# Optimization experiments

Hardware: AMD Instinct MI355X
Metric: run time of the kernel (lower is better)

## Reference

```python
import jax, jax.numpy as jnp
import numpy as np

HIDDEN = 128

def setup_inputs() -> dict:
    key = jax.random.key(0)
    ks = jax.random.split(key, 7)
    B, T, I, O = 256, 512, 256, 1000
    s_ih = 1.0 / np.sqrt(HIDDEN)
    x = jax.random.normal(ks[0], (B, T, I), dtype=jnp.float32)
    W_ih = jax.random.uniform(ks[1], (HIDDEN, I), minval=-s_ih, maxval=s_ih, dtype=jnp.float32)
    W_hh = jax.random.uniform(ks[2], (HIDDEN, HIDDEN), minval=-s_ih, maxval=s_ih, dtype=jnp.float32)
    b_ih = jax.random.uniform(ks[3], (HIDDEN,), minval=-s_ih, maxval=s_ih, dtype=jnp.float32)
    b_hh = jax.random.uniform(ks[4], (HIDDEN,), minval=-s_ih, maxval=s_ih, dtype=jnp.float32)
    s_fc = 1.0 / np.sqrt(HIDDEN)
    W_fc = jax.random.uniform(ks[5], (O, HIDDEN), minval=-s_fc, maxval=s_fc, dtype=jnp.float32)
    b_fc = jax.random.uniform(ks[6], (O,), minval=-s_fc, maxval=s_fc, dtype=jnp.float32)
    return {"x": x, "W_ih": W_ih, "W_hh": W_hh, "b_ih": b_ih, "b_hh": b_hh, "W_fc": W_fc, "b_fc": b_fc}


def reference(x, W_ih, W_hh, b_ih, b_hh, W_fc, b_fc):
    B = x.shape[0]
    # Precompute input projection for all timesteps in one big GEMM: [B,T,H]
    xp = jnp.einsum('bti,hi->bth', x, W_ih) + b_ih + b_hh
    h0 = jnp.zeros((B, HIDDEN), dtype=x.dtype)

    def step(h, xp_t):
        h = jnp.tanh(xp_t + h @ W_hh.T)
        return h, None

    # scan over time axis; only the final hidden state feeds the fc head
    h_last, _ = jax.lax.scan(step, h0, jnp.swapaxes(xp, 0, 1))
    return h_last @ W_fc.T + b_fc
```

## Files before the change

### kernel.cpp

```cpp
#include <hip/hip_runtime.h>


#define HID    128
#define TSTEPS 512
#define BATCH  256
#define INDIM  256
#define ODIM   1000

typedef _Float16 f16x8 __attribute__((ext_vector_type(8)));
typedef __fp16   fp16x2 __attribute__((ext_vector_type(2)));
typedef float    f32x4 __attribute__((ext_vector_type(4)));

__device__ __forceinline__ unsigned pk16(float a, float b) {
    union { fp16x2 h; unsigned u; } t;
    t.h = __builtin_amdgcn_cvt_pkrtz(a, b);
    return t.u;
}
__device__ __forceinline__ float tanh_fast(float v) {
    float e = __expf(2.f * v);
    float r = __builtin_amdgcn_rcpf(e + 1.f);
    return __builtin_fmaf(-2.f, r, 1.f);
}

__global__ __launch_bounds__(256) void k_phase1(const float* __restrict__ x,
                                                const float* __restrict__ Wih,
                                                const float* __restrict__ bih,
                                                const float* __restrict__ bhh,
                                                float* __restrict__ xp) {
    __shared__ __align__(16) _Float16 xs[2][4096];
    __shared__ __align__(16) _Float16 wsm[2][4096];

    const int tid  = threadIdx.x;
    const int wave = tid >> 6, lane = tid & 63;
    const int quad = lane >> 4, l16 = lane & 15;
    const int wm = wave >> 1, wn = wave & 1;
    const int m0 = blockIdx.x * 128;

    int srow[4], scol[4], sdst[4];
#pragma unroll
    for (int q = 0; q < 4; q++) {
        int li = q * 256 + tid;
        srow[q] = li >> 3;
        scol[q] = li & 7;
        sdst[q] = srow[q] * 32 + ((((scol[q] >> 1) ^ srow[q]) & 3) << 3) + ((scol[q] & 1) << 2);
    }

    f32x4 bias_v[4];
#pragma unroll
    for (int nt = 0; nt < 4; nt++) {
        int j0 = wn * 64 + nt * 16 + quad * 4;
        bias_v[nt] = *(const f32x4*)(bih + j0) + *(const f32x4*)(bhh + j0);
    }

    float4 rx[4], rw[4];
#define LOAD_STAGE(KC)                                                              \
    {                                                                               \
        _Pragma("unroll") for (int q = 0; q < 4; q++) {                             \
            rx[q] = *(const float4*)(x + (size_t)(m0 + srow[q]) * INDIM + (KC) * 32 + scol[q] * 4); \
            rw[q] = *(const float4*)(Wih + (size_t)srow[q] * INDIM + (KC) * 32 + scol[q] * 4);      \
        }                                                                           \
    }
#define WRITE_STAGE(BUF)                                                            \
    {                                                                               \
        _Pragma("unroll") for (int q = 0; q < 4; q++) {                             \
            uint2 px, pw;                                                           \
            px.x = pk16(rx[q].x, rx[q].y); px.y = pk16(rx[q].z, rx[q].w);           \
            pw.x = pk16(rw[q].x, rw[q].y); pw.y = pk16(rw[q].z, rw[q].w);           \
            *(uint2*)&xs[BUF][sdst[q]]  = px;                                       \
            *(uint2*)&wsm[BUF][sdst[q]] = pw;                                       \
        }                                                                           \
    }

    f32x4 acc[4][4];
#pragma unroll
    for (int mt = 0; mt < 4; mt++)
#pragma unroll
        for (int nt = 0; nt < 4; nt++) {
            acc[mt][nt].x = 0.f; acc[mt][nt].y = 0.f;
            acc[mt][nt].z = 0.f; acc[mt][nt].w = 0.f;
        }

    LOAD_STAGE(0);
    WRITE_STAGE(0);
    __syncthreads();

    for (int kc = 0; kc < 8; kc++) {
        const int b = kc & 1;
        if (kc < 7) LOAD_STAGE(kc + 1);

        f16x8 a[4], bw[4];
#pragma unroll
        for (int mt = 0; mt < 4; mt++) {
            int row = wm * 64 + mt * 16 + l16;
            a[mt] = *(const f16x8*)&xs[b][row * 32 + (((quad ^ row) & 3) << 3)];
        }
#pragma unroll
        for (int nt = 0; nt < 4; nt++) {
            int row = wn * 64 + nt * 16 + l16;
            bw[nt] = *(const f16x8*)&wsm[b][row * 32 + (((quad ^ row) & 3) << 3)];
        }
#pragma unroll
        for (int mt = 0; mt < 4; mt++)
#pragma unroll
            for (int nt = 0; nt < 4; nt++)
                acc[mt][nt] = __builtin_amdgcn_mfma_f32_16x16x32_f16(bw[nt], a[mt], acc[mt][nt], 0, 0, 0);

        if (kc < 7) WRITE_STAGE(b ^ 1);
        __syncthreads();
    }

#pragma unroll
    for (int mt = 0; mt < 4; mt++) {
        int row = m0 + wm * 64 + mt * 16 + l16;
#pragma unroll
        for (int nt = 0; nt < 4; nt++) {
            int col = wn * 64 + nt * 16 + quad * 4;
            *(f32x4*)&xp[(size_t)row * HID + col] = acc[mt][nt] + bias_v[nt];
        }
    }
#undef LOAD_STAGE
#undef WRITE_STAGE
}

#define RNN_STEP4(TV, XQI, XQC, PB) {                                             \
    uint2 pw;                                                                     \
    pw.x = pk16(tanh_fast(C.x), tanh_fast(C.y));                                  \
    pw.y = pk16(tanh_fast(C.z), tanh_fast(C.w));                                  \
    *(uint2*)&hp[PB][waddr] = pw;                                                 \
    if ((TV) + 4 < TSTEPS)                                                        \
        XQI = *(const f32x4*)(xpb + ((TV) + 4) * HID);                            \
    asm volatile("s_waitcnt lgkmcnt(0)\n\ts_barrier" ::: "memory");               \
    f16x8 H0 = *(const f16x8*)&hp[PB][raddr0];                                    \
    f16x8 H1 = *(const f16x8*)&hp[PB][raddr1];                                    \
    f16x8 H2 = *(const f16x8*)&hp[PB][raddr2];                                    \
    f16x8 H3 = *(const f16x8*)&hp[PB][raddr3];                                    \
    f32x4 ch = XQC, cl;                                                           \
    cl.x = 0.f; cl.y = 0.f; cl.z = 0.f; cl.w = 0.f;                               \
    ch = __builtin_amdgcn_mfma_f32_16x16x32_f16(Wf[0], H0, ch, 0, 0, 0);          \
    cl = __builtin_amdgcn_mfma_f32_16x16x32_f16(Wf[2], H2, cl, 0, 0, 0);          \
    ch = __builtin_amdgcn_mfma_f32_16x16x32_f16(Wf[1], H1, ch, 0, 0, 0);          \
    cl = __builtin_amdgcn_mfma_f32_16x16x32_f16(Wf[3], H3, cl, 0, 0, 0);          \
    C = ch + cl;                                                                  \
}

__global__ __launch_bounds__(512) void k_rnn4(const float* __restrict__ Whh,
                                              float* __restrict__ ws) {
    __shared__ __align__(16) _Float16 hp[2][16 * 128];
    const int tid  = threadIdx.x;
    const int wave = tid >> 6, lane = tid & 63;
    const int quad = lane >> 4, l16 = lane & 15;
    const int r0   = blockIdx.x * 16;

    f16x8 Wf[4];
#pragma unroll
    for (int kc = 0; kc < 4; kc++) {
        const float* p = Whh + (size_t)(16 * wave + l16) * HID + kc * 32 + quad * 8;
        float4 e0 = *(const float4*)p, e1 = *(const float4*)(p + 4);
        union { unsigned u[4]; f16x8 v; } t;
        t.u[0] = pk16(e0.x, e0.y); t.u[1] = pk16(e0.z, e0.w);
        t.u[2] = pk16(e1.x, e1.y); t.u[3] = pk16(e1.z, e1.w);
        Wf[kc] = t.v;
    }

    const int raddr0 = l16 * 128 + ((((0 * 4 + quad) ^ l16) & 15) << 3);
    const int raddr1 = l16 * 128 + ((((1 * 4 + quad) ^ l16) & 15) << 3);
    const int raddr2 = l16 * 128 + ((((2 * 4 + quad) ^ l16) & 15) << 3);
    const int raddr3 = l16 * 128 + ((((3 * 4 + quad) ^ l16) & 15) << 3);
    const int waddr  = l16 * 128 + ((((2 * wave + (quad >> 1)) ^ l16) & 15) << 3) + ((quad & 1) << 2);

    const float* xpb = ws + (size_t)(r0 + l16) * (TSTEPS * HID) + 16 * wave + 4 * quad;

    f32x4 C, xq0, xq1, xq2, xq3;
    C   = *(const f32x4*)(xpb);
    xq1 = *(const f32x4*)(xpb + 1 * HID);
    xq2 = *(const f32x4*)(xpb + 2 * HID);
    xq3 = *(const f32x4*)(xpb + 3 * HID);

    for (int t = 0; t < 508; t += 4) {
        RNN_STEP4(t,     xq0, xq1, 0);
        RNN_STEP4(t + 1, xq1, xq2, 1);
        RNN_STEP4(t + 2, xq2, xq3, 0);
        RNN_STEP4(t + 3, xq3, xq0, 1);
    }
    RNN_STEP4(508, xq0, xq1, 0);
    RNN_STEP4(509, xq1, xq2, 1);
    RNN_STEP4(510, xq2, xq3, 0);

    f32x4 o;
    o.x = tanh_fast(C.x); o.y = tanh_fast(C.y);
    o.z = tanh_fast(C.z); o.w = tanh_fast(C.w);
    *(f32x4*)(ws + (size_t)(r0 + l16) * (TSTEPS * HID) + 16 * wave + 4 * quad) = o;
}
#undef RNN_STEP4

__global__ __launch_bounds__(256) void k_fc(const float* __restrict__ ws,
                                            const float* __restrict__ Wfc,
                                            const float* __restrict__ bfc,
                                            float* __restrict__ out) {
    __shared__ float hb[HID];
    const int b   = blockIdx.x;
    const int tid = threadIdx.x;
    if (tid < HID) hb[tid] = ws[(size_t)b * (TSTEPS * HID) + tid];
    __syncthreads();

    for (int o = tid; o < ODIM; o += 256) {
        const float* wr = Wfc + (size_t)o * HID;
        float acc = 0.f;
#pragma unroll
        for (int q = 0; q < 32; q++) {
            float4 wv = *(const float4*)(wr + q * 4);
            float4 hv = *(const float4*)&hb[q * 4];
            acc += wv.x * hv.x + wv.y * hv.y + wv.z * hv.z + wv.w * hv.w;
        }
        out[(size_t)b * ODIM + o] = acc + bfc[o];
    }
}

extern "C" void kernel_launch(void* const* d_in, const int* in_sizes, int n_in,
                              void* d_out, int out_size, void* d_ws, size_t ws_size,
                              hipStream_t stream) {
    const float* x   = (const float*)d_in[0];
    const float* Wih = (const float*)d_in[1];
    const float* Whh = (const float*)d_in[2];
    const float* bih = (const float*)d_in[3];
    const float* bhh = (const float*)d_in[4];
    const float* Wfc = (const float*)d_in[5];
    const float* bfc = (const float*)d_in[6];
    float* out = (float*)d_out;
    float* ws  = (float*)d_ws;

    k_phase1<<<dim3(1024), dim3(256), 0, stream>>>(x, Wih, bih, bhh, ws);
    k_rnn4  <<<dim3(16),   dim3(512), 0, stream>>>(Whh, ws);
    k_fc    <<<dim3(BATCH), dim3(256), 0, stream>>>(ws, Wfc, bfc, out);
}
```

Before: 375.4 us.

## Fuse input projection and recurrence with staged atomic counters and fp16 workspace

Merges the input-projection GEMM and the recurrent scan into one launch. Sixteen blocks run the recurrence while the remaining blocks compute the projection in four time-ordered stages, each signalled through a global atomic counter, so the scan can start before the full GEMM finishes. The projected activations are also stored in fp16 rather than fp32, halving workspace traffic. The cost is reduced precision of the precomputed inputs, and the spin-wait relies on all recurrence blocks being co-resident with the producers, which risks stalls or deadlock if scheduling does not cooperate.

```diff
diff --git a/kernel.cpp b/kernel.cpp
--- a/kernel.cpp
+++ b/kernel.cpp
@@ -22,134 +22,133 @@
     return __builtin_fmaf(-2.f, r, 1.f);
 }
 
-__global__ __launch_bounds__(256) void k_phase1(const float* __restrict__ x,
-                                                const float* __restrict__ Wih,
-                                                const float* __restrict__ bih,
-                                                const float* __restrict__ bhh,
-                                                float* __restrict__ xp) {
+#define CTR_OFF (33u << 20)
+
+__global__ void k_zero(float* ws) {
+    int* ctr = (int*)((char*)ws + CTR_OFF);
+    if (threadIdx.x < 4) ctr[threadIdx.x] = 0;
+}
+
+
+__global__ __launch_bounds__(512) void k_fused(const float* __restrict__ x,
+                                               const float* __restrict__ Wih,
+                                               const float* __restrict__ bih,
+                                               const float* __restrict__ bhh,
+                                               const float* __restrict__ Whh,
+                                               float* __restrict__ ws) {
     __shared__ __align__(16) _Float16 xs[2][4096];
     __shared__ __align__(16) _Float16 wsm[2][4096];
+    __shared__ __align__(16) _Float16 hp[2][16 * 128];
 
     const int tid  = threadIdx.x;
     const int wave = tid >> 6, lane = tid & 63;
     const int quad = lane >> 4, l16 = lane & 15;
-    const int wm = wave >> 1, wn = wave & 1;
-    const int m0 = blockIdx.x * 128;
-
-    int srow[4], scol[4], sdst[4];
-#pragma unroll
-    for (int q = 0; q < 4; q++) {
-        int li = q * 256 + tid;
-        srow[q] = li >> 3;
-        scol[q] = li & 7;
-        sdst[q] = srow[q] * 32 + ((((scol[q] >> 1) ^ srow[q]) & 3) << 3) + ((scol[q] & 1) << 2);
-    }
-
-    f32x4 bias_v[4];
-#pragma unroll
-    for (int nt = 0; nt < 4; nt++) {
-        int j0 = wn * 64 + nt * 16 + quad * 4;
-        bias_v[nt] = *(const f32x4*)(bih + j0) + *(const f32x4*)(bhh + j0);
-    }
-
-    float4 rx[4], rw[4];
+    int* ctr = (int*)((char*)ws + CTR_OFF);
+    _Float16* xp16 = (_Float16*)ws;
+
+    if (blockIdx.x >= 16) {
+        const int pb    = blockIdx.x - 16;
+        const int stage = pb >> 8;
+        const int m0    = ((pb & 255) * 4 + stage) * 128;
+        const int wm = wave >> 1, wn = wave & 1;
+
+        int srow[2], scol[2], sdst[2];
+#pragma unroll
+        for (int q = 0; q < 2; q++) {
+            int li = q * 512 + tid;
+            srow[q] = li >> 3;
+            scol[q] = li & 7;
+            sdst[q] = srow[q] * 32 + ((((scol[q] >> 1) ^ srow[q]) & 3) << 3) + ((scol[q] & 1) << 2);
+        }
+
+        f32x4 bias_v[4];
+#pragma unroll
+        for (int nt = 0; nt < 4; nt++) {
+            int j0 = wn * 64 + nt * 16 + quad * 4;
+            bias_v[nt] = *(const f32x4*)(bih + j0) + *(const f32x4*)(bhh + j0);
+        }
+
+        float4 rx[2], rw[2];
 #define LOAD_STAGE(KC)                                                              \
-    {                                                                               \
-        _Pragma("unroll") for (int q = 0; q < 4; q++) {                             \
-            rx[q] = *(const float4*)(x + (size_t)(m0 + srow[q]) * INDIM + (KC) * 32 + scol[q] * 4); \
-            rw[q] = *(const float4*)(Wih + (size_t)srow[q] * INDIM + (KC) * 32 + scol[q] * 4);      \
-        }                                                                           \
-    }
+        {                                                                           \
+            _Pragma("unroll") for (int q = 0; q < 2; q++) {                         \
+                rx[q] = *(const float4*)(x + (size_t)(m0 + srow[q]) * INDIM + (KC) * 32 + scol[q] * 4); \
+                rw[q] = *(const float4*)(Wih + (size_t)srow[q] * INDIM + (KC) * 32 + scol[q] * 4);      \
+            }                                                                       \
+        }
 #define WRITE_STAGE(BUF)                                                            \
-    {                                                                               \
-        _Pragma("unroll") for (int q = 0; q < 4; q++) {                             \
-            uint2 px, pw;                                                           \
-            px.x = pk16(rx[q].x, rx[q].y); px.y = pk16(rx[q].z, rx[q].w);           \
-            pw.x = pk16(rw[q].x, rw[q].y); pw.y = pk16(rw[q].z, rw[q].w);           \
-            *(uint2*)&xs[BUF][sdst[q]]  = px;                                       \
-            *(uint2*)&wsm[BUF][sdst[q]] = pw;                                       \
-        }                                                                           \
-    }
-
-    f32x4 acc[4][4];
-#pragma unroll
-    for (int mt = 0; mt < 4; mt++)
-#pragma unroll
-        for (int nt = 0; nt < 4; nt++) {
-            acc[mt][nt].x = 0.f; acc[mt][nt].y = 0.f;
-            acc[mt][nt].z = 0.f; acc[mt][nt].w = 0.f;
-        }
-
-    LOAD_STAGE(0);
-    WRITE_STAGE(0);
-    __syncthreads();
-
-    for (int kc = 0; kc < 8; kc++) {
-        const int b = kc & 1;
-        if (kc < 7) LOAD_STAGE(kc + 1);
-
-        f16x8 a[4], bw[4];
-#pragma unroll
-        for (int mt = 0; mt < 4; mt++) {
-            int row = wm * 64 + mt * 16 + l16;
-            a[mt] = *(const f16x8*)&xs[b][row * 32 + (((quad ^ row) & 3) << 3)];
-        }
-#pragma unroll
-        for (int nt = 0; nt < 4; nt++) {
-            int row = wn * 64 + nt * 16 + l16;
-            bw[nt] = *(const f16x8*)&wsm[b][row * 32 + (((quad ^ row) & 3) << 3)];
-        }
-#pragma unroll
-        for (int mt = 0; mt < 4; mt++)
-#pragma unroll
-            for (int nt = 0; nt < 4; nt++)
-                acc[mt][nt] = __builtin_amdgcn_mfma_f32_16x16x32_f16(bw[nt], a[mt], acc[mt][nt], 0, 0, 0);
-
-        if (kc < 7) WRITE_STAGE(b ^ 1);
+        {                                                                           \
+            _Pragma("unroll") for (int q = 0; q < 2; q++) {                         \
+                uint2 px, pw;                                                       \
+                px.x = pk16(rx[q].x, rx[q].y); px.y = pk16(rx[q].z, rx[q].w);       \
+                pw.x = pk16(rw[q].x, rw[q].y); pw.y = pk16(rw[q].z, rw[q].w);       \
+                *(uint2*)&xs[BUF][sdst[q]]  = px;                                   \
+                *(uint2*)&wsm[BUF][sdst[q]] = pw;                                   \
+            }                                                                       \
+        }
+
+        f32x4 acc[2][4];
+#pragma unroll
+        for (int mt = 0; mt < 2; mt++)
+#pragma unroll
+            for (int nt = 0; nt < 4; nt++) {
+                acc[mt][nt].x = 0.f; acc[mt][nt].y = 0.f;
+                acc[mt][nt].z = 0.f; acc[mt][nt].w = 0.f;
+            }
+
+        LOAD_STAGE(0);
+        WRITE_STAGE(0);
         __syncthreads();
-    }
-
-#pragma unroll
-    for (int mt = 0; mt < 4; mt++) {
-        int row = m0 + wm * 64 + mt * 16 + l16;
-#pragma unroll
-        for (int nt = 0; nt < 4; nt++) {
-            int col = wn * 64 + nt * 16 + quad * 4;
-            *(f32x4*)&xp[(size_t)row * HID + col] = acc[mt][nt] + bias_v[nt];
-        }
-    }
+
+        for (int kc = 0; kc < 8; kc++) {
+            const int b = kc & 1;
+            if (kc < 7) LOAD_STAGE(kc + 1);
+
+            f16x8 a[2], bw[4];
+#pragma unroll
+            for (int mt = 0; mt < 2; mt++) {
+                int row = wm * 32 + mt * 16 + l16;
+                a[mt] = *(const f16x8*)&xs[b][row * 32 + (((quad ^ row) & 3) << 3)];
+            }
+#pragma unroll
+            for (int nt = 0; nt < 4; nt++) {
+                int row = wn * 64 + nt * 16 + l16;
+                bw[nt] = *(const f16x8*)&wsm[b][row * 32 + (((quad ^ row) & 3) << 3)];
+            }
+#pragma unroll
+            for (int mt = 0; mt < 2; mt++)
+#pragma unroll
+                for (int nt = 0; nt < 4; nt++)
+                    acc[mt][nt] = __builtin_amdgcn_mfma_f32_16x16x32_f16(bw[nt], a[mt], acc[mt][nt], 0, 0, 0);
+
+            if (kc < 7) WRITE_STAGE(b ^ 1);
+            __syncthreads();
+        }
+
+#pragma unroll
+        for (int mt = 0; mt < 2; mt++) {
+            int row = m0 + wm * 32 + mt * 16 + l16;
+#pragma unroll
+            for (int nt = 0; nt < 4; nt++) {
+                int col = wn * 64 + nt * 16 + quad * 4;
+                f32x4 v = acc[mt][nt] + bias_v[nt];
+                uint2 p;
+                p.x = pk16(v.x, v.y); p.y = pk16(v.z, v.w);
+                *(uint2*)&xp16[(size_t)row * HID + col] = p;
+            }
+        }
 #undef LOAD_STAGE
 #undef WRITE_STAGE
-}
-
-#define RNN_STEP4(TV, XQI, XQC, PB) {                                             \
-    uint2 pw;                                                                     \
-    pw.x = pk16(tanh_fast(C.x), tanh_fast(C.y));                                  \
-    pw.y = pk16(tanh_fast(C.z), tanh_fast(C.w));                                  \
-    *(uint2*)&hp[PB][waddr] = pw;                                                 \
-    if ((TV) + 4 < TSTEPS)                                                        \
-        XQI = *(const f32x4*)(xpb + ((TV) + 4) * HID);                            \
-    asm volatile("s_waitcnt lgkmcnt(0)\n\ts_barrier" ::: "memory");               \
-    f16x8 H0 = *(const f16x8*)&hp[PB][raddr0];                                    \
-    f16x8 H1 = *(const f16x8*)&hp[PB][raddr1];                                    \
-    f16x8 H2 = *(const f16x8*)&hp[PB][raddr2];                                    \
-    f16x8 H3 = *(const f16x8*)&hp[PB][raddr3];                                    \
-    f32x4 ch = XQC, cl;                                                           \
-    cl.x = 0.f; cl.y = 0.f; cl.z = 0.f; cl.w = 0.f;                               \
-    ch = __builtin_amdgcn_mfma_f32_16x16x32_f16(Wf[0], H0, ch, 0, 0, 0);          \
-    cl = __builtin_amdgcn_mfma_f32_16x16x32_f16(Wf[2], H2, cl, 0, 0, 0);          \
-    ch = __builtin_amdgcn_mfma_f32_16x16x32_f16(Wf[1], H1, ch, 0, 0, 0);          \
-    cl = __builtin_amdgcn_mfma_f32_16x16x32_f16(Wf[3], H3, cl, 0, 0, 0);          \
-    C = ch + cl;                                                                  \
-}
-
-__global__ __launch_bounds__(512) void k_rnn4(const float* __restrict__ Whh,
-                                              float* __restrict__ ws) {
-    __shared__ __align__(16) _Float16 hp[2][16 * 128];
-    const int tid  = threadIdx.x;
-    const int wave = tid >> 6, lane = tid & 63;
-    const int quad = lane >> 4, l16 = lane & 15;
-    const int r0   = blockIdx.x * 16;
+
+        __syncthreads();
+        if (tid == 0) {
+            __threadfence();
+            atomicAdd(&ctr[stage], 1);
+        }
+        return;
+    }
+
+    const int r0 = blockIdx.x * 16;
 
     f16x8 Wf[4];
 #pragma unroll
@@ -168,30 +167,102 @@
     const int raddr3 = l16 * 128 + ((((3 * 4 + quad) ^ l16) & 15) << 3);
     const int waddr  = l16 * 128 + ((((2 * wave + (quad >> 1)) ^ l16) & 15) << 3) + ((quad & 1) << 2);
 
-    const float* xpb = ws + (size_t)(r0 + l16) * (TSTEPS * HID) + 16 * wave + 4 * quad;
-
-    f32x4 C, xq0, xq1, xq2, xq3;
-    C   = *(const f32x4*)(xpb);
-    xq1 = *(const f32x4*)(xpb + 1 * HID);
-    xq2 = *(const f32x4*)(xpb + 2 * HID);
-    xq3 = *(const f32x4*)(xpb + 3 * HID);
-
-    for (int t = 0; t < 508; t += 4) {
+    const _Float16* xpb = xp16 + (size_t)(r0 + l16) * (TSTEPS * HID) + 16 * wave + 4 * quad;
+
+#define WAITSTAGE(S)                                                                \
+    {                                                                               \
+        if (tid == 0) {                                                             \
+            long iv = 0;                                                            \
+            while (__hip_atomic_load(&ctr[S], __ATOMIC_ACQUIRE,                     \
+                                     __HIP_MEMORY_SCOPE_AGENT) < 256 &&             \
+                   ++iv < 200000000L) {}                                            \
+        }                                                                           \
+        __syncthreads();                                                            \
+        __threadfence();                                                            \
+    }
+
+#define CVT4(DST, SRC)                                                              \
+    {                                                                               \
+        union { uint2 u; _Float16 h[4]; } cv_; cv_.u = (SRC);                       \
+        DST.x = (float)cv_.h[0]; DST.y = (float)cv_.h[1];                           \
+        DST.z = (float)cv_.h[2]; DST.w = (float)cv_.h[3];                           \
+    }
+
+#define RNN_STEP4(TV, XQI, XQC, PB) {                                             \
+    uint2 pw;                                                                     \
+    pw.x = pk16(tanh_fast(C.x), tanh_fast(C.y));                                  \
+    pw.y = pk16(tanh_fast(C.z), tanh_fast(C.w));                                  \
+    *(uint2*)&hp[PB][waddr] = pw;                                                 \
+    if ((TV) + 4 < TSTEPS)                                                        \
+        XQI = *(const uint2*)(xpb + (size_t)((TV) + 4) * HID);                    \
+    asm volatile("s_waitcnt lgkmcnt(0)\n\ts_barrier" ::: "memory");               \
+    f32x4 ch; CVT4(ch, XQC);                        \
+    f16x8 H0 = *(const f16x8*)&hp[PB][raddr0];                                    \
+    f16x8 H1 = *(const f16x8*)&hp[PB][raddr1];                                    \
+    f16x8 H2 = *(const f16x8*)&hp[PB][raddr2];                                    \
+    f16x8 H3 = *(const f16x8*)&hp[PB][raddr3];                                    \
+    f32x4 cl;                                                                     \
+    cl.x = 0.f; cl.y = 0.f; cl.z = 0.f; cl.w = 0.f;                               \
+    ch = __builtin_amdgcn_mfma_f32_16x16x32_f16(Wf[0], H0, ch, 0, 0, 0);          \
+    cl = __builtin_amdgcn_mfma_f32_16x16x32_f16(Wf[2], H2, cl, 0, 0, 0);          \
+    ch = __builtin_amdgcn_mfma_f32_16x16x32_f16(Wf[1], H1, ch, 0, 0, 0);          \
+    cl = __builtin_amdgcn_mfma_f32_16x16x32_f16(Wf[3], H3, cl, 0, 0, 0);          \
+    C = ch + cl;                                                                  \
+}
+
+    WAITSTAGE(0);
+
+    f32x4 C;
+    uint2 xq0, xq1, xq2, xq3;
+    {
+        uint2 c0 = *(const uint2*)(xpb);
+        CVT4(C, c0);
+    }
+    xq1 = *(const uint2*)(xpb + 1 * HID);
+    xq2 = *(const uint2*)(xpb + 2 * HID);
+    xq3 = *(const uint2*)(xpb + 3 * HID);
+
+    for (int t = 0; t < 124; t += 4) {
         RNN_STEP4(t,     xq0, xq1, 0);
         RNN_STEP4(t + 1, xq1, xq2, 1);
         RNN_STEP4(t + 2, xq2, xq3, 0);
         RNN_STEP4(t + 3, xq3, xq0, 1);
     }
+    WAITSTAGE(1);
+    for (int t = 124; t < 252; t += 4) {
+        RNN_STEP4(t,     xq0, xq1, 0);
+        RNN_STEP4(t + 1, xq1, xq2, 1);
+        RNN_STEP4(t + 2, xq2, xq3, 0);
+        RNN_STEP4(t + 3, xq3, xq0, 1);
+    }
+    WAITSTAGE(2);
+    for (int t = 252; t < 380; t += 4) {
+        RNN_STEP4(t,     xq0, xq1, 0);
+        RNN_STEP4(t + 1, xq1, xq2, 1);
+        RNN_STEP4(t + 2, xq2, xq3, 0);
+        RNN_STEP4(t + 3, xq3, xq0, 1);
+    }
+    WAITSTAGE(3);
+    for (int t = 380; t < 508; t += 4) {
+        RNN_STEP4(t,     xq0, xq1, 0);
+        RNN_STEP4(t + 1, xq1, xq2, 1);
+        RNN_STEP4(t + 2, xq2, xq3, 0);
+        RNN_STEP4(t + 3, xq3, xq0, 1);
+    }
     RNN_STEP4(508, xq0, xq1, 0);
     RNN_STEP4(509, xq1, xq2, 1);
     RNN_STEP4(510, xq2, xq3, 0);
 
-    f32x4 o;
-    o.x = tanh_fast(C.x); o.y = tanh_fast(C.y);
-    o.z = tanh_fast(C.z); o.w = tanh_fast(C.w);
-    *(f32x4*)(ws + (size_t)(r0 + l16) * (TSTEPS * HID) + 16 * wave + 4 * quad) = o;
-}
+    {
+        uint2 p;
+        p.x = pk16(tanh_fast(C.x), tanh_fast(C.y));
+        p.y = pk16(tanh_fast(C.z), tanh_fast(C.w));
+        *(uint2*)(xp16 + (size_t)(r0 + l16) * (TSTEPS * HID) + 16 * wave + 4 * quad) = p;
+    }
 #undef RNN_STEP4
+#undef CVT4
+#undef WAITSTAGE
+}
 
 __global__ __launch_bounds__(256) void k_fc(const float* __restrict__ ws,
                                             const float* __restrict__ Wfc,
@@ -200,7 +271,8 @@
     __shared__ float hb[HID];
     const int b   = blockIdx.x;
     const int tid = threadIdx.x;
-    if (tid < HID) hb[tid] = ws[(size_t)b * (TSTEPS * HID) + tid];
+    const _Float16* xp16 = (const _Float16*)ws;
+    if (tid < HID) hb[tid] = (float)xp16[(size_t)b * (TSTEPS * HID) + tid];
     __syncthreads();
 
     for (int o = tid; o < ODIM; o += 256) {
@@ -229,7 +301,7 @@
     float* out = (float*)d_out;
     float* ws  = (float*)d_ws;
 
-    k_phase1<<<dim3(1024), dim3(256), 0, stream>>>(x, Wih, bih, bhh, ws);
-    k_rnn4  <<<dim3(16),   dim3(512), 0, stream>>>(Whh, ws);
-    k_fc    <<<dim3(BATCH), dim3(256), 0, stream>>>(ws, Wfc, bfc, out);
-}
+    k_zero <<<dim3(1),    dim3(64),  0, stream>>>(ws);
+    k_fused<<<dim3(1040), dim3(512), 0, stream>>>(x, Wih, bih, bhh, Whh, ws);
+    k_fc   <<<dim3(BATCH), dim3(256), 0, stream>>>(ws, Wfc, bfc, out);
+}
```

Measured after the change: 441.9 us. 1.18x slower.
